# Performance work log

Hardware: AMD Instinct MI355X
Metric: run time of the kernel (lower is better)

Reference implementation:

```python
import jax, jax.numpy as jnp
from jax import lax
import numpy as np

B, T, D, U = 32, 2048, 256, 256


def setup_inputs() -> dict:
    key = jax.random.key(0)
    k1, k2, k3 = jax.random.split(key, 3)
    scale_x = 1.0 / np.sqrt(D)
    scale_h = 1.0 / np.sqrt(U)
    return {
        "data": jax.random.normal(k1, (B, T, D), dtype=jnp.float32),
        "Wx": jax.random.normal(k2, (D, 4 * U), dtype=jnp.float32) * scale_x,
        "Wh": jax.random.normal(k3, (U, 4 * U), dtype=jnp.float32) * scale_h,
        "b": jnp.zeros((4 * U,), dtype=jnp.float32),
    }


def reference(data, Wx, Wh, b):
    # data: [B, T, D] -> LSTM with zero initial hidden/cell state,
    # return_sequences=True -> outputs [B, T, U].
    Bq, Tq, _ = data.shape
    Uq = Wh.shape[0]
    # Precompute the input projection for all timesteps in one big GEMM.
    zx = jnp.einsum("btd,dk->btk", data, Wx) + b  # [B, T, 4U]
    zx_t = jnp.swapaxes(zx, 0, 1)  # [T, B, 4U] for scan over time

    def step(carry, zx_step):
        h, c = carry
        z = zx_step + h @ Wh  # [B, 4U]
        i, f, g, o = jnp.split(z, 4, axis=-1)
        c = jax.nn.sigmoid(f) * c + jax.nn.sigmoid(i) * jnp.tanh(g)
        h = jax.nn.sigmoid(o) * jnp.tanh(c)
        return (h, c), h

    h0 = jnp.zeros((Bq, Uq), dtype=data.dtype)
    c0 = jnp.zeros((Bq, Uq), dtype=data.dtype)
    (_, _), hs = lax.scan(step, (h0, c0), zx_t)  # hs: [T, B, U]
    return jnp.swapaxes(hs, 0, 1)  # [B, T, U]
```

## Files before the change

### kernel.cpp

```cpp
#include <hip/hip_runtime.h>
#include <hip/hip_bf16.h>

#define Tn 2048
#define Bn 32
#define Dn 256
#define Un 256
#define NBLK 16

using short8 = __attribute__((ext_vector_type(8))) short;
using f32x4  = __attribute__((ext_vector_type(4))) float;
using int4v  = __attribute__((ext_vector_type(4))) int;

__device__ __forceinline__ unsigned short f2bf(float f) {
    unsigned int u = __builtin_bit_cast(unsigned int, f);
    u += 0x7fffu + ((u >> 16) & 1u);
    return (unsigned short)(u >> 16);
}
__device__ __forceinline__ float bf2f(unsigned short v) {
    unsigned int u = ((unsigned int)v) << 16;
    return __builtin_bit_cast(float, u);
}
__device__ __forceinline__ float rcp_f(float x) { return __builtin_amdgcn_rcpf(x); }
__device__ __forceinline__ float sigm(float x)   { return rcp_f(1.0f + __expf(-x)); }
__device__ __forceinline__ float tanh_f(float x) { return 1.0f - 2.0f * rcp_f(__expf(2.0f * x) + 1.0f); }

__global__ __launch_bounds__(512) void gemm_zx(const float* __restrict__ data,
                                               const float* __restrict__ Wx,
                                               unsigned short* __restrict__ zws)
{
    __shared__ unsigned short BsubT[128 * 40];

    const int bid = blockIdx.x;
    const int bn = bid & 7;
    const int bm = bid >> 3;
    const int tid = threadIdx.x;
    const int lane = tid & 63, wid = tid >> 6;
    const int wm = wid >> 2, wn = wid & 3;
    const int l15 = lane & 15, lk = lane >> 4;

    f32x4 acc[4][2];
    #pragma unroll
    for (int mt = 0; mt < 4; ++mt)
        #pragma unroll
        for (int nt = 0; nt < 2; ++nt)
            acc[mt][nt] = f32x4{0.f, 0.f, 0.f, 0.f};

    const int colStage = tid & 127;
    const int kqStage  = tid >> 7;

    for (int ks = 0; ks < 8; ++ks) {
        __syncthreads();
        {
            const float* wp = Wx + (size_t)(ks * 32 + kqStage) * 1024 + bn * 128 + colStage;
            #pragma unroll
            for (int kk = 0; kk < 8; ++kk) {
                float v = wp[(size_t)kk * 4 * 1024];
                BsubT[colStage * 40 + (kqStage + kk * 4)] = f2bf(v);
            }
        }
        __syncthreads();

        short8 afr[4];
        #pragma unroll
        for (int mt = 0; mt < 4; ++mt) {
            int row = bm * 128 + wm * 64 + mt * 16 + l15;
            const float* ap = data + (size_t)row * 256 + ks * 32 + lk * 8;
            float4 a0 = *(const float4*)(ap);
            float4 a1 = *(const float4*)(ap + 4);
            short8 a;
            a[0] = (short)f2bf(a0.x); a[1] = (short)f2bf(a0.y);
            a[2] = (short)f2bf(a0.z); a[3] = (short)f2bf(a0.w);
            a[4] = (short)f2bf(a1.x); a[5] = (short)f2bf(a1.y);
            a[6] = (short)f2bf(a1.z); a[7] = (short)f2bf(a1.w);
            afr[mt] = a;
        }
        #pragma unroll
        for (int nt = 0; nt < 2; ++nt) {
            int colL = wn * 32 + nt * 16 + l15;
            short8 bfr = *(const short8*)&BsubT[colL * 40 + lk * 8];
            #pragma unroll
            for (int mt = 0; mt < 4; ++mt)
                acc[mt][nt] = __builtin_amdgcn_mfma_f32_16x16x32_bf16(afr[mt], bfr, acc[mt][nt], 0, 0, 0);
        }
    }

    #pragma unroll
    for (int mt = 0; mt < 4; ++mt) {
        #pragma unroll
        for (int nt = 0; nt < 2; ++nt) {
            int col = bn * 128 + wn * 32 + nt * 16 + l15;
            #pragma unroll
            for (int r = 0; r < 4; ++r) {
                int row = bm * 128 + wm * 64 + mt * 16 + lk * 4 + r;
                int b_ = row >> 11;
                int t_ = row & 2047;
                zws[(size_t)(t_ * 32 + b_) * 1024 + col] = f2bf(acc[mt][nt][r]);
            }
        }
    }
}

__global__ void wh_transpose(const float* __restrict__ Wh,
                             unsigned short* __restrict__ WhT)
{
    const int c = blockIdx.x;
    const int k = threadIdx.x;
    WhT[c * 256 + k] = f2bf(Wh[(size_t)k * 1024 + c]);
}

__global__ __launch_bounds__(128) void lstm_rec(
    const unsigned short* __restrict__ WhT,
    const float* __restrict__ bias,
    const unsigned short* __restrict__ zws,
    unsigned short* __restrict__ hG,
    unsigned int* __restrict__ flagB,
    float* __restrict__ out)
{
    const int chunk = blockIdx.x;
    const int tid = threadIdx.x;
    const int lane = tid & 63;
    const int mt = tid >> 6;
    const int l15 = lane & 15, lk = lane >> 4;

    const int u = chunk * 16 + l15;

    short8 Bf[4][8];
    #pragma unroll
    for (int g = 0; g < 4; ++g)
        #pragma unroll
        for (int ks = 0; ks < 8; ++ks)
            Bf[g][ks] = *(const short8*)(WhT + (size_t)(g * 256 + u) * 256 + ks * 32 + lk * 8);

    float bias_r[4];
    #pragma unroll
    for (int g = 0; g < 4; ++g) bias_r[g] = bias[g * 256 + u];

    float c_state[4];
    #pragma unroll
    for (int r = 0; r < 4; ++r) c_state[r] = 0.0f;

    unsigned short zx_pf[4][4];
    #pragma unroll
    for (int g = 0; g < 4; ++g)
        #pragma unroll
        for (int r = 0; r < 4; ++r)
            zx_pf[g][r] = zws[(size_t)(mt * 16 + lk * 4 + r) * 1024 + g * 256 + u];

    for (int t = 0; t < Tn; ++t) {
        f32x4 acc[4];
        #pragma unroll
        for (int g = 0; g < 4; ++g) acc[g] = f32x4{0.f, 0.f, 0.f, 0.f};

        if (t > 0) {
            const unsigned int* fp = flagB + (size_t)(lane & 15) * 32;
            unsigned int v;
            do {
                v = __hip_atomic_load(fp, __ATOMIC_RELAXED, __HIP_MEMORY_SCOPE_AGENT);
            } while (!__all((int)(v >= (unsigned int)t)));

            const unsigned short* hp = hG + (size_t)((t - 1) & 1) * (32 * 256);
            int4v Afr[8];
            #pragma unroll
            for (int ks = 0; ks < 8; ++ks) {
                unsigned long long aaddr =
                    (unsigned long long)(hp + (size_t)(mt * 16 + l15) * 256 + ks * 32 + lk * 8);
                asm volatile("global_load_dwordx4 %0, %1, off sc0 sc1"
                             : "=v"(Afr[ks]) : "v"(aaddr) : "memory");
            }
            asm volatile("s_waitcnt vmcnt(0)" ::: "memory");
            __builtin_amdgcn_sched_barrier(0);

            #pragma unroll
            for (int ks = 0; ks < 8; ++ks) {
                short8 af = __builtin_bit_cast(short8, Afr[ks]);
                #pragma unroll
                for (int g = 0; g < 4; ++g)
                    acc[g] = __builtin_amdgcn_mfma_f32_16x16x32_bf16(af, Bf[g][ks], acc[g], 0, 0, 0);
            }
        }

        float hval[4];
        #pragma unroll
        for (int r = 0; r < 4; ++r) {
            const float zi = acc[0][r] + bf2f(zx_pf[0][r]) + bias_r[0];
            const float zf = acc[1][r] + bf2f(zx_pf[1][r]) + bias_r[1];
            const float zg = acc[2][r] + bf2f(zx_pf[2][r]) + bias_r[2];
            const float zo = acc[3][r] + bf2f(zx_pf[3][r]) + bias_r[3];
            const float ig = sigm(zi), fg = sigm(zf);
            const float gg = tanh_f(zg), og = sigm(zo);
            const float cs = fg * c_state[r] + ig * gg;
            c_state[r] = cs;
            hval[r] = og * tanh_f(cs);
        }

        unsigned short* hw = hG + (size_t)(t & 1) * (32 * 256);
        #pragma unroll
        for (int r = 0; r < 4; ++r) {
            const int b = mt * 16 + lk * 4 + r;
            unsigned long long haddr = (unsigned long long)(hw + (size_t)b * 256 + u);
            unsigned int hb = (unsigned int)f2bf(hval[r]);
            asm volatile("global_store_short %0, %1, off sc0 sc1"
                         :: "v"(haddr), "v"(hb) : "memory");
        }
        asm volatile("s_waitcnt vmcnt(0)" ::: "memory");
        __syncthreads();
        if (tid == 0)
            __hip_atomic_store(&flagB[(size_t)chunk * 32], (unsigned int)(t + 1),
                               __ATOMIC_RELAXED, __HIP_MEMORY_SCOPE_AGENT);

        #pragma unroll
        for (int r = 0; r < 4; ++r) {
            const int b = mt * 16 + lk * 4 + r;
            out[(size_t)b * (Tn * Un) + (size_t)t * Un + u] = hval[r];
        }
        if (t + 1 < Tn) {
            #pragma unroll
            for (int g = 0; g < 4; ++g)
                #pragma unroll
                for (int r = 0; r < 4; ++r)
                    zx_pf[g][r] = zws[((size_t)(t + 1) * 32 + mt * 16 + lk * 4 + r) * 1024
                                      + g * 256 + u];
        }
    }
}

extern "C" void kernel_launch(void* const* d_in, const int* in_sizes, int n_in,
                              void* d_out, int out_size, void* d_ws, size_t ws_size,
                              hipStream_t stream)
{
    const float* data = (const float*)d_in[0];
    const float* Wx   = (const float*)d_in[1];
    const float* Wh   = (const float*)d_in[2];
    const float* bias = (const float*)d_in[3];
    float* out = (float*)d_out;

    char* ws = (char*)d_ws;
    unsigned short* zws = (unsigned short*)ws;
    size_t off = (size_t)Tn * Bn * 1024 * 2;
    unsigned short* WhT = (unsigned short*)(ws + off);
    off += (size_t)1024 * 256 * 2;
    unsigned short* hG = (unsigned short*)(ws + off);
    off += (size_t)2 * 32 * 256 * 2;
    unsigned int* flagB = (unsigned int*)(ws + off);

    hipMemsetAsync(flagB, 0, NBLK * 32 * sizeof(unsigned int), stream);

    wh_transpose<<<dim3(1024), dim3(256), 0, stream>>>(Wh, WhT);
    gemm_zx<<<dim3(4096), dim3(512), 0, stream>>>(data, Wx, zws);
    lstm_rec<<<dim3(NBLK), dim3(128), 0, stream>>>(WhT, bias, zws, hG, flagB, out);
}
```

Measured before the change: 5.320 ms.

## Replace flag-based barrier with tagged hidden-state words and fewer wider blocks

Each hidden value is now stored as a 32-bit word with a step tag in the upper half. Consumers poll the h buffer directly and check that the tags sum to the expected value, which removes the separate flag store, the __syncthreads and the flag-polling round trip. The recurrence runs on 8 blocks of 256 threads instead of 16 blocks of 128, and the output store and zx prefetch are deferred and double-buffered two steps ahead. The cost is twice the bytes per h read, repeated full-buffer reloads while polling, and extra unpacking work before the MFMAs.

```diff
diff --git a/kernel.cpp b/kernel.cpp
--- a/kernel.cpp
+++ b/kernel.cpp
@@ -5,11 +5,12 @@
 #define Bn 32
 #define Dn 256
 #define Un 256
-#define NBLK 16
+#define NBLK 8
 
 using short8 = __attribute__((ext_vector_type(8))) short;
 using f32x4  = __attribute__((ext_vector_type(4))) float;
 using int4v  = __attribute__((ext_vector_type(4))) int;
+using u16x2  = __attribute__((ext_vector_type(2))) unsigned short;
 
 __device__ __forceinline__ unsigned short f2bf(float f) {
     unsigned int u = __builtin_bit_cast(unsigned int, f);
@@ -108,21 +109,24 @@
     WhT[c * 256 + k] = f2bf(Wh[(size_t)k * 1024 + c]);
 }
 
-__global__ __launch_bounds__(128) void lstm_rec(
+struct ZxRegs { unsigned short v[4][4]; };
+
+__global__ __launch_bounds__(256, 1) void lstm_rec(
     const unsigned short* __restrict__ WhT,
     const float* __restrict__ bias,
     const unsigned short* __restrict__ zws,
-    unsigned short* __restrict__ hG,
-    unsigned int* __restrict__ flagB,
+    unsigned int* __restrict__ hT,
     float* __restrict__ out)
 {
     const int chunk = blockIdx.x;
-    const int tid = threadIdx.x;
+    const int tid  = threadIdx.x;
     const int lane = tid & 63;
-    const int mt = tid >> 6;
-    const int l15 = lane & 15, lk = lane >> 4;
-
-    const int u = chunk * 16 + l15;
+    const int wid  = tid >> 6;
+    const int wm   = wid >> 1;
+    const int wn   = wid & 1;
+    const int l15  = lane & 15, lk = lane >> 4;
+
+    const int u = chunk * 32 + wn * 16 + l15;
 
     short8 Bf[4][8];
     #pragma unroll
@@ -139,88 +143,123 @@
     #pragma unroll
     for (int r = 0; r < 4; ++r) c_state[r] = 0.0f;
 
-    unsigned short zx_pf[4][4];
+    ZxRegs zxE, zxO;
     #pragma unroll
     for (int g = 0; g < 4; ++g)
         #pragma unroll
-        for (int r = 0; r < 4; ++r)
-            zx_pf[g][r] = zws[(size_t)(mt * 16 + lk * 4 + r) * 1024 + g * 256 + u];
-
-    for (int t = 0; t < Tn; ++t) {
-        f32x4 acc[4];
-        #pragma unroll
-        for (int g = 0; g < 4; ++g) acc[g] = f32x4{0.f, 0.f, 0.f, 0.f};
-
-        if (t > 0) {
-            const unsigned int* fp = flagB + (size_t)(lane & 15) * 32;
-            unsigned int v;
-            do {
-                v = __hip_atomic_load(fp, __ATOMIC_RELAXED, __HIP_MEMORY_SCOPE_AGENT);
-            } while (!__all((int)(v >= (unsigned int)t)));
-
-            const unsigned short* hp = hG + (size_t)((t - 1) & 1) * (32 * 256);
-            int4v Afr[8];
-            #pragma unroll
-            for (int ks = 0; ks < 8; ++ks) {
-                unsigned long long aaddr =
-                    (unsigned long long)(hp + (size_t)(mt * 16 + l15) * 256 + ks * 32 + lk * 8);
-                asm volatile("global_load_dwordx4 %0, %1, off sc0 sc1"
-                             : "=v"(Afr[ks]) : "v"(aaddr) : "memory");
-            }
-            asm volatile("s_waitcnt vmcnt(0)" ::: "memory");
-            __builtin_amdgcn_sched_barrier(0);
-
-            #pragma unroll
-            for (int ks = 0; ks < 8; ++ks) {
-                short8 af = __builtin_bit_cast(short8, Afr[ks]);
-                #pragma unroll
-                for (int g = 0; g < 4; ++g)
-                    acc[g] = __builtin_amdgcn_mfma_f32_16x16x32_bf16(af, Bf[g][ks], acc[g], 0, 0, 0);
-            }
-        }
-
-        float hval[4];
-        #pragma unroll
         for (int r = 0; r < 4; ++r) {
-            const float zi = acc[0][r] + bf2f(zx_pf[0][r]) + bias_r[0];
-            const float zf = acc[1][r] + bf2f(zx_pf[1][r]) + bias_r[1];
-            const float zg = acc[2][r] + bf2f(zx_pf[2][r]) + bias_r[2];
-            const float zo = acc[3][r] + bf2f(zx_pf[3][r]) + bias_r[3];
+            zxE.v[g][r] = zws[(size_t)(0 * 32 + wm * 16 + lk * 4 + r) * 1024 + g * 256 + u];
+            zxO.v[g][r] = zws[(size_t)(1 * 32 + wm * 16 + lk * 4 + r) * 1024 + g * 256 + u];
+        }
+
+    float hprev[4];
+
+    auto gates_publish = [&](int t, const ZxRegs& cur, const f32x4* acc) {
+        unsigned int* hw = hT + (size_t)(t & 1) * (Bn * Un);
+        #pragma unroll
+        for (int r = 0; r < 4; ++r) {
+            const float zi = acc[0][r] + bf2f(cur.v[0][r]) + bias_r[0];
+            const float zf = acc[1][r] + bf2f(cur.v[1][r]) + bias_r[1];
+            const float zg = acc[2][r] + bf2f(cur.v[2][r]) + bias_r[2];
+            const float zo = acc[3][r] + bf2f(cur.v[3][r]) + bias_r[3];
             const float ig = sigm(zi), fg = sigm(zf);
             const float gg = tanh_f(zg), og = sigm(zo);
             const float cs = fg * c_state[r] + ig * gg;
             c_state[r] = cs;
-            hval[r] = og * tanh_f(cs);
-        }
-
-        unsigned short* hw = hG + (size_t)(t & 1) * (32 * 256);
+            const float h = og * tanh_f(cs);
+
+            const int b = wm * 16 + lk * 4 + r;
+            unsigned long long haddr = (unsigned long long)(hw + (size_t)b * 256 + u);
+            unsigned int dw = ((unsigned int)(t + 1) << 16) | (unsigned int)f2bf(h);
+            asm volatile("global_store_dword %0, %1, off sc0 sc1"
+                         :: "v"(haddr), "v"(dw) : "memory");
+            hprev[r] = h;
+        }
+    };
+
+    auto step = [&](int t, ZxRegs& zxUse) {
+        const unsigned int* hb = hT + (size_t)((t - 1) & 1) * (Bn * Un)
+                                    + (size_t)(wm * 16 + l15) * 256;
+        const unsigned short target = (unsigned short)(64u * (unsigned int)t);
+        int4v tg[16];
+        while (true) {
+            #pragma unroll
+            for (int ks = 0; ks < 8; ++ks) {
+                unsigned long long a0 = (unsigned long long)(hb + ks * 32 + lk * 8);
+                asm volatile("global_load_dwordx4 %0, %1, off sc0 sc1"
+                             : "=v"(tg[2 * ks]) : "v"(a0) : "memory");
+                asm volatile("global_load_dwordx4 %0, %1, off sc0 sc1"
+                             : "=v"(tg[2 * ks + 1]) : "v"(a0 + 16) : "memory");
+            }
+            asm volatile("s_waitcnt vmcnt(0)" ::: "memory");
+            __builtin_amdgcn_sched_barrier(0);
+            u16x2 s = {0, 0};
+            #pragma unroll
+            for (int i = 0; i < 16; ++i)
+                #pragma unroll
+                for (int j = 0; j < 4; ++j)
+                    s += __builtin_bit_cast(u16x2, tg[i][j]);
+            if (__all((int)(s[1] == target))) break;
+        }
+        __builtin_amdgcn_sched_barrier(0);
+
         #pragma unroll
         for (int r = 0; r < 4; ++r) {
-            const int b = mt * 16 + lk * 4 + r;
-            unsigned long long haddr = (unsigned long long)(hw + (size_t)b * 256 + u);
-            unsigned int hb = (unsigned int)f2bf(hval[r]);
-            asm volatile("global_store_short %0, %1, off sc0 sc1"
-                         :: "v"(haddr), "v"(hb) : "memory");
-        }
-        asm volatile("s_waitcnt vmcnt(0)" ::: "memory");
-        __syncthreads();
-        if (tid == 0)
-            __hip_atomic_store(&flagB[(size_t)chunk * 32], (unsigned int)(t + 1),
-                               __ATOMIC_RELAXED, __HIP_MEMORY_SCOPE_AGENT);
-
-        #pragma unroll
-        for (int r = 0; r < 4; ++r) {
-            const int b = mt * 16 + lk * 4 + r;
-            out[(size_t)b * (Tn * Un) + (size_t)t * Un + u] = hval[r];
-        }
-        if (t + 1 < Tn) {
+            const int b = wm * 16 + lk * 4 + r;
+            out[(size_t)b * (Tn * Un) + (size_t)(t - 1) * Un + u] = hprev[r];
+        }
+        ZxRegs cur = zxUse;
+        if (t + 2 < Tn) {
             #pragma unroll
             for (int g = 0; g < 4; ++g)
                 #pragma unroll
                 for (int r = 0; r < 4; ++r)
-                    zx_pf[g][r] = zws[((size_t)(t + 1) * 32 + mt * 16 + lk * 4 + r) * 1024
-                                      + g * 256 + u];
-        }
+                    zxUse.v[g][r] = zws[((size_t)(t + 2) * 32 + wm * 16 + lk * 4 + r) * 1024
+                                        + g * 256 + u];
+        }
+
+        f32x4 acc[4];
+        #pragma unroll
+        for (int g = 0; g < 4; ++g) acc[g] = f32x4{0.f, 0.f, 0.f, 0.f};
+        #pragma unroll
+        for (int ks = 0; ks < 8; ++ks) {
+            int4v p;
+            p[0] = (int)((((unsigned)tg[2 * ks][1]) << 16)     | ((unsigned)tg[2 * ks][0]     & 0xffffu));
+            p[1] = (int)((((unsigned)tg[2 * ks][3]) << 16)     | ((unsigned)tg[2 * ks][2]     & 0xffffu));
+            p[2] = (int)((((unsigned)tg[2 * ks + 1][1]) << 16) | ((unsigned)tg[2 * ks + 1][0] & 0xffffu));
+            p[3] = (int)((((unsigned)tg[2 * ks + 1][3]) << 16) | ((unsigned)tg[2 * ks + 1][2] & 0xffffu));
+            short8 af = __builtin_bit_cast(short8, p);
+            #pragma unroll
+            for (int g = 0; g < 4; ++g)
+                acc[g] = __builtin_amdgcn_mfma_f32_16x16x32_bf16(af, Bf[g][ks], acc[g], 0, 0, 0);
+        }
+
+        gates_publish(t, cur, acc);
+    };
+
+    {
+        f32x4 acc0[4];
+        #pragma unroll
+        for (int g = 0; g < 4; ++g) acc0[g] = f32x4{0.f, 0.f, 0.f, 0.f};
+        ZxRegs cur = zxE;
+        #pragma unroll
+        for (int g = 0; g < 4; ++g)
+            #pragma unroll
+            for (int r = 0; r < 4; ++r)
+                zxE.v[g][r] = zws[((size_t)2 * 32 + wm * 16 + lk * 4 + r) * 1024 + g * 256 + u];
+        gates_publish(0, cur, acc0);
+    }
+
+    for (int t = 1; t + 1 < Tn; t += 2) {
+        step(t,     zxO);
+        step(t + 1, zxE);
+    }
+    step(Tn - 1, zxO);
+
+    #pragma unroll
+    for (int r = 0; r < 4; ++r) {
+        const int b = wm * 16 + lk * 4 + r;
+        out[(size_t)b * (Tn * Un) + (size_t)(Tn - 1) * Un + u] = hprev[r];
     }
 }
 
@@ -239,13 +278,11 @@
     size_t off = (size_t)Tn * Bn * 1024 * 2;
     unsigned short* WhT = (unsigned short*)(ws + off);
     off += (size_t)1024 * 256 * 2;
-    unsigned short* hG = (unsigned short*)(ws + off);
-    off += (size_t)2 * 32 * 256 * 2;
-    unsigned int* flagB = (unsigned int*)(ws + off);
-
-    hipMemsetAsync(flagB, 0, NBLK * 32 * sizeof(unsigned int), stream);
+    unsigned int* hT = (unsigned int*)(ws + off);
+
+    hipMemsetAsync(hT, 0, (size_t)2 * Bn * Un * sizeof(unsigned int), stream);
 
     wh_transpose<<<dim3(1024), dim3(256), 0, stream>>>(Wh, WhT);
     gemm_zx<<<dim3(4096), dim3(512), 0, stream>>>(data, Wx, zws);
-    lstm_rec<<<dim3(NBLK), dim3(128), 0, stream>>>(WhT, bias, zws, hG, flagB, out);
-}
+    lstm_rec<<<dim3(NBLK), dim3(256), 0, stream>>>(WhT, bias, zws, hT, out);
+}
```

After: 9.493 ms. +78.4%, slower.
